# Kernel optimization log

Hardware: AMD Instinct MI355X
Metric: run time of the kernel (lower is better)

The kernel has to match this reference:

```python
import jax, jax.numpy as jnp
import numpy as np

B, T, S, H, NH, F = 16, 512, 512, 1024, 16, 4096
HD = H // NH


def _mha(x, bias, mem, wq, bq, wk, bk, wv, bv, wo, bo):
    # THUMT MultiHeadAttention: q scaled by head_dim**-0.5, additive bias on logits
    b, t, h = x.shape
    q = (x @ wq + bq) * (HD ** -0.5)
    k = mem @ wk + bk
    v = mem @ wv + bv
    split = lambda z: z.reshape(z.shape[0], z.shape[1], NH, HD).transpose(0, 2, 1, 3)
    logits = jnp.einsum('bhqd,bhkd->bhqk', split(q), split(k)) + bias
    w = jax.nn.softmax(logits, axis=-1)
    o = jnp.einsum('bhqk,bhkd->bhqd', w, split(v))
    o = o.transpose(0, 2, 1, 3).reshape(b, t, h)
    return o @ wo + bo


def _lstm(inp, w, b):
    # inp: [B, T, 2H]; gates affine over concat([x_t, h], -1): [3H] -> [4H]
    bsz = inp.shape[0]
    def step(carry, xt):
        c, hdd = carry
        g = jnp.concatenate([xt, hdd], axis=-1) @ w + b
        i, j, f, o = jnp.split(g, 4, axis=-1)
        new_c = jax.nn.sigmoid(f) * c + jax.nn.sigmoid(i) * jnp.tanh(j)
        new_h = jax.nn.sigmoid(o) * jnp.tanh(new_c)
        return (new_c, new_h), new_h
    init = (jnp.zeros((bsz, H), inp.dtype), jnp.zeros((bsz, H), inp.dtype))
    _, hs = jax.lax.scan(step, init, inp.transpose(1, 0, 2))  # [T,B,H]
    return hs.transpose(1, 0, 2)


def setup_inputs() -> dict:
    key = jax.random.key(0)
    ks = jax.random.split(key, 16)
    d = {}
    d['x'] = jax.random.normal(ks[0], (B, T, H), jnp.float32)
    d['memory'] = jax.random.normal(ks[1], (B, S, H), jnp.float32)
    d['src_bias'] = jnp.zeros((B, 1, 1, S), jnp.float32)
    causal = jnp.triu(jnp.full((T, T), -1e9, jnp.float32), k=1)
    d['tgt_bias'] = causal[None, None]
    sc = 0.02
    names = ['src_wq', 'src_wk', 'src_wv', 'src_wo', 'tgt_wq', 'tgt_wk', 'tgt_wv', 'tgt_wo']
    for i, n in enumerate(names):
        d[n] = jax.random.normal(ks[2 + i], (H, H), jnp.float32) * sc
        d[n.replace('w', 'b')] = jnp.zeros((H,), jnp.float32)
    d['lstm_w'] = jax.random.normal(ks[10], (3 * H, 4 * H), jnp.float32) * sc
    d['lstm_b'] = jnp.zeros((4 * H,), jnp.float32)
    d['ffn_w1'] = jax.random.normal(ks[11], (H, F), jnp.float32) * sc
    d['ffn_b1'] = jnp.zeros((F,), jnp.float32)
    d['ffn_w2'] = jax.random.normal(ks[12], (F, H), jnp.float32) * sc
    d['ffn_b2'] = jnp.zeros((H,), jnp.float32)
    return d


def reference(x, memory, src_bias, tgt_bias,
              src_wq, src_bq, src_wk, src_bk, src_wv, src_bv, src_wo, src_bo,
              tgt_wq, tgt_bq, tgt_wk, tgt_bk, tgt_wv, tgt_bv, tgt_wo, tgt_bo,
              lstm_w, lstm_b, ffn_w1, ffn_b1, ffn_w2, ffn_b2):
    c_src = _mha(x, src_bias, memory, src_wq, src_bq, src_wk, src_bk, src_wv, src_bv, src_wo, src_bo)
    c_tgt = _mha(x, tgt_bias, x, tgt_wq, tgt_bq, tgt_wk, tgt_bk, tgt_wv, tgt_bv, tgt_wo, tgt_bo)
    c = c_src + c_tgt  # comb_mode='sum'
    hiddens = _lstm(jnp.concatenate([x, c], axis=-1), lstm_w, lstm_b)
    hiddens = jax.nn.relu(hiddens @ ffn_w1 + ffn_b1) @ ffn_w2 + ffn_b2  # FeedForward
    return hiddens  # dropout is identity in eval
```

## Files before the change

### kernel.cpp

```cpp
#include <hip/hip_runtime.h>
#include <hip/hip_bf16.h>
#include <stdint.h>


typedef unsigned short u16;
typedef unsigned int u32;
typedef unsigned long long u64;
typedef __bf16 bf16x8 __attribute__((ext_vector_type(8)));
typedef float f32x4 __attribute__((ext_vector_type(4)));
typedef int int32x4 __attribute__((ext_vector_type(4)));
typedef unsigned long long u64x2 __attribute__((ext_vector_type(2)));

#define DEV static __device__ __forceinline__

DEV u16 f2bf(float x) {
  u32 u = __builtin_bit_cast(u32, x);
  u += 0x7FFF + ((u >> 16) & 1);
  return (u16)(u >> 16);
}

DEV bf16x8 ldfrag(const void* p) {
  int32x4 v = *(const int32x4*)p;
  return __builtin_bit_cast(bf16x8, v);
}

DEV bf16x8 mkfrag(u64 lo, u64 hi) {
  u64x2 v;
  v.x = lo;
  v.y = hi;
  return __builtin_bit_cast(bf16x8, v);
}

DEV f32x4 mfma_bf16(bf16x8 a, bf16x8 b, f32x4 c) {
  return __builtin_amdgcn_mfma_f32_16x16x32_bf16(a, b, c, 0, 0, 0);
}

DEV void load_lds16(const u16* g, u16* l) {
  __builtin_amdgcn_global_load_lds(
      (__attribute__((address_space(1))) void*)(uintptr_t)g,
      (__attribute__((address_space(3))) void*)(uintptr_t)l, 16, 0, 0);
}


__global__ __launch_bounds__(256) void cvt_bf16_kernel(u16* __restrict__ out,
                                                       const float* __restrict__ in,
                                                       int n4) {
  int i = blockIdx.x * 256 + threadIdx.x;
  if (i >= n4) return;
  float4 v = ((const float4*)in)[i];
  ushort4 s;
  s.x = f2bf(v.x); s.y = f2bf(v.y); s.z = f2bf(v.z); s.w = f2bf(v.w);
  ((ushort4*)out)[i] = s;
}

__global__ __launch_bounds__(256) void cvt_x_kernel(u16* __restrict__ out,
                                                    const float* __restrict__ in) {
  int i = blockIdx.x * 256 + threadIdx.x;
  int r = i >> 8, cg4 = i & 255;
  float4 v = ((const float4*)in)[i];
  ushort4 s;
  s.x = f2bf(v.x); s.y = f2bf(v.y); s.z = f2bf(v.z); s.w = f2bf(v.w);
  *(ushort4*)(out + (size_t)r * 2048 + cg4 * 4) = s;
}

__global__ __launch_bounds__(256) void convt_kernel(u16* __restrict__ out,
                                                    const float* __restrict__ in,
                                                    int K, int N, int koff, float scale) {
  __shared__ float tile[32][33];
  const int tid = threadIdx.x;
  const int n0 = blockIdx.x * 32, k0 = blockIdx.y * 32;
  const int c = tid & 31, r = tid >> 5;
#pragma unroll
  for (int i = 0; i < 4; ++i)
    tile[r + i * 8][c] = in[(size_t)(k0 + r + i * 8 + koff) * N + n0 + c];
  __syncthreads();
#pragma unroll
  for (int i = 0; i < 4; ++i)
    out[(size_t)(n0 + r + i * 8) * K + k0 + c] = f2bf(tile[c][r + i * 8] * scale);
}

__global__ __launch_bounds__(256) void convt_perm_kernel(u16* __restrict__ out,
                                                         const float* __restrict__ in,
                                                         int K, int koff) {
  __shared__ float tile[32][33];
  const int tid = threadIdx.x;
  const int u0 = blockIdx.x * 32, k0 = blockIdx.y * 32, g = blockIdx.z;
  const int c = tid & 31, r = tid >> 5;
#pragma unroll
  for (int i = 0; i < 4; ++i)
    tile[r + i * 8][c] = in[(size_t)(k0 + r + i * 8 + koff) * 4096 + g * 1024 + u0 + c];
  __syncthreads();
#pragma unroll
  for (int i = 0; i < 4; ++i)
    out[(size_t)((u0 + r + i * 8) * 4 + g) * K + k0 + c] = f2bf(tile[c][r + i * 8]);
}

__global__ __launch_bounds__(256) void pack_bias_kernel(float* __restrict__ out,
                                                        const float* __restrict__ in) {
  int p = blockIdx.x * 256 + threadIdx.x;
  out[p] = in[(p & 3) * 1024 + (p >> 2)];
}

template <int OUTBF, int ACCUM, int RELU, int PERM>
__global__ __launch_bounds__(256) void gemm_bt_kernel(
    const u16* __restrict__ A, int lda, const u16* __restrict__ Bt,
    const float* __restrict__ bias, float bscale,
    void* __restrict__ outp, int ostride,
    const float* __restrict__ cacc, int cstride, int K) {
  __shared__ u16 As[128 * 32];
  __shared__ u16 Bs[128 * 32];
  const int tid = threadIdx.x;
  const int wave = tid >> 6, lane = tid & 63;
  const int lr = lane & 15, lg = lane >> 4;
  const int m0 = blockIdx.y * 128, n0 = blockIdx.x * 128;
  const int wr = (wave >> 1) * 64, wc = (wave & 1) * 64;

  f32x4 acc[4][4] = {};

  const int sr = lane >> 2, sce = (lane & 3) * 8;
  const u16* gA = A + (size_t)(m0 + wave * 16 + sr) * lda + sce;
  const u16* gB = Bt + (size_t)(n0 + wave * 16 + sr) * K + sce;
  u16* lA = As + wave * 16 * 32;
  u16* lB = Bs + wave * 16 * 32;

  for (int k0 = 0; k0 < K; k0 += 32) {
    __syncthreads();
    load_lds16(gA + k0, lA);
    load_lds16(gA + k0 + (size_t)64 * lda, lA + 64 * 32);
    load_lds16(gB + k0, lB);
    load_lds16(gB + k0 + (size_t)64 * K, lB + 64 * 32);
    __syncthreads();
    bf16x8 af[4], bfr[4];
    const u16* pa = As + (wr + lr) * 32 + lg * 8;
    const u16* pb = Bs + (wc + lr) * 32 + lg * 8;
#pragma unroll
    for (int i = 0; i < 4; ++i) af[i] = ldfrag(pa + i * 16 * 32);
#pragma unroll
    for (int j = 0; j < 4; ++j) bfr[j] = ldfrag(pb + j * 16 * 32);
#pragma unroll
    for (int i = 0; i < 4; ++i)
#pragma unroll
      for (int j = 0; j < 4; ++j)
        acc[i][j] = mfma_bf16(af[i], bfr[j], acc[i][j]);
  }

  const int col0 = n0 + wc + lr;
  const int row0 = m0 + wr + lg * 4;
#pragma unroll
  for (int i = 0; i < 4; ++i) {
#pragma unroll
    for (int j = 0; j < 4; ++j) {
      const int c = col0 + j * 16;
      const float bv = bias ? bias[c] * bscale : 0.f;
#pragma unroll
      for (int ii = 0; ii < 4; ++ii) {
        const int r = row0 + i * 16 + ii;
        float v = acc[i][j][ii] + bv;
        if (ACCUM) v += cacc[(size_t)r * cstride + c];
        if (RELU) v = fmaxf(v, 0.f);
        const int rp = (PERM == 2) ? ((r & 15) * 512 + (r >> 4)) : r;
        if (OUTBF) ((u16*)outp)[(size_t)rp * ostride + c] = f2bf(v);
        else       ((float*)outp)[(size_t)rp * ostride + c] = v;
      }
    }
  }
}

template <int CAUSAL>
__global__ __launch_bounds__(256) void flash_kernel(
    const u16* __restrict__ Q, const u16* __restrict__ Kb, const u16* __restrict__ Vb,
    const float* __restrict__ sbias, u16* __restrict__ O) {
  __shared__ u16 Kl[64 * 72];
  __shared__ u16 Vt[64 * 72];
  __shared__ u16 Pl[64 * 72];
  const int tid = threadIdx.x, wave = tid >> 6, lane = tid & 63;
  const int lr = lane & 15, lg = lane >> 4;
  const int q0 = blockIdx.x * 64, hh = blockIdx.y, b = blockIdx.z;

  bf16x8 qf[2];
  {
    const u16* qp = Q + (size_t)(b * 512 + q0 + wave * 16 + lr) * 1024 + hh * 64 + lg * 8;
    qf[0] = ldfrag(qp);
    qf[1] = ldfrag(qp + 32);
  }
  f32x4 oacc[4] = {};
  float mrun[4], lsum[4];
#pragma unroll
  for (int ii = 0; ii < 4; ++ii) { mrun[ii] = -3e38f; lsum[ii] = 0.f; }

  const int ntiles = CAUSAL ? (q0 / 64 + 1) : 8;
  for (int ti = 0; ti < ntiles; ++ti) {
    const int s0 = ti * 64;
    {
      const int r = tid >> 2, ch = (tid & 3) * 16;
      const u16* kp = Kb + (size_t)(b * 512 + s0 + r) * 1024 + hh * 64 + ch;
      const u16* vp = Vb + (size_t)(b * 512 + s0 + r) * 1024 + hh * 64 + ch;
      int32x4 k0v = *(const int32x4*)kp;
      int32x4 k1v = *(const int32x4*)(kp + 8);
      int32x4 v0v = *(const int32x4*)vp;
      int32x4 v1v = *(const int32x4*)(vp + 8);
      *(int32x4*)&Kl[r * 72 + ch] = k0v;
      *(int32x4*)&Kl[r * 72 + ch + 8] = k1v;
      const u16* v0p = (const u16*)&v0v;
      const u16* v1p = (const u16*)&v1v;
#pragma unroll
      for (int j = 0; j < 8; ++j) {
        Vt[(ch + j) * 72 + r] = v0p[j];
        Vt[(ch + 8 + j) * 72 + r] = v1p[j];
      }
    }
    __syncthreads();
    f32x4 sf[4] = {};
#pragma unroll
    for (int j = 0; j < 4; ++j)
#pragma unroll
      for (int ks = 0; ks < 2; ++ks) {
        bf16x8 kf = ldfrag(&Kl[(j * 16 + lr) * 72 + ks * 32 + lg * 8]);
        sf[j] = mfma_bf16(qf[ks], kf, sf[j]);
      }
    if (!CAUSAL) {
#pragma unroll
      for (int j = 0; j < 4; ++j) {
        const float bv = sbias[b * 512 + s0 + j * 16 + lr];
#pragma unroll
        for (int ii = 0; ii < 4; ++ii) sf[j][ii] += bv;
      }
    } else {
#pragma unroll
      for (int j = 0; j < 4; ++j) {
        const int s = s0 + j * 16 + lr;
#pragma unroll
        for (int ii = 0; ii < 4; ++ii) {
          const int q = q0 + wave * 16 + lg * 4 + ii;
          if (s > q) sf[j][ii] -= 1e9f;
        }
      }
    }
    float sc[4], rs[4];
#pragma unroll
    for (int ii = 0; ii < 4; ++ii) {
      float m = fmaxf(fmaxf(sf[0][ii], sf[1][ii]), fmaxf(sf[2][ii], sf[3][ii]));
#pragma unroll
      for (int off = 1; off < 16; off <<= 1) m = fmaxf(m, __shfl_xor(m, off));
      const float mn = fmaxf(mrun[ii], m);
      sc[ii] = __expf(mrun[ii] - mn);
      mrun[ii] = mn;
      rs[ii] = 0.f;
    }
#pragma unroll
    for (int j = 0; j < 4; ++j)
#pragma unroll
      for (int ii = 0; ii < 4; ++ii) {
        const float p = __expf(sf[j][ii] - mrun[ii]);
        rs[ii] += p;
        Pl[(wave * 16 + lg * 4 + ii) * 72 + j * 16 + lr] = f2bf(p);
      }
#pragma unroll
    for (int ii = 0; ii < 4; ++ii) {
      float r = rs[ii];
#pragma unroll
      for (int off = 1; off < 16; off <<= 1) r += __shfl_xor(r, off);
      lsum[ii] = lsum[ii] * sc[ii] + r;
    }
#pragma unroll
    for (int df = 0; df < 4; ++df)
#pragma unroll
      for (int ii = 0; ii < 4; ++ii) oacc[df][ii] *= sc[ii];
    __syncthreads();
    bf16x8 pf[2];
    pf[0] = ldfrag(&Pl[(wave * 16 + lr) * 72 + lg * 8]);
    pf[1] = ldfrag(&Pl[(wave * 16 + lr) * 72 + 32 + lg * 8]);
#pragma unroll
    for (int df = 0; df < 4; ++df)
#pragma unroll
      for (int ks = 0; ks < 2; ++ks) {
        bf16x8 vf = ldfrag(&Vt[(df * 16 + lr) * 72 + ks * 32 + lg * 8]);
        oacc[df] = mfma_bf16(pf[ks], vf, oacc[df]);
      }
    __syncthreads();
  }
#pragma unroll
  for (int df = 0; df < 4; ++df)
#pragma unroll
    for (int ii = 0; ii < 4; ++ii) {
      const float v = oacc[df][ii] / lsum[ii];
      O[(size_t)(b * 512 + q0 + wave * 16 + lg * 4 + ii) * 1024 + hh * 64 + df * 16 + lr] =
          f2bf(v);
    }
}

#define SCAN_NW 32
__global__ __launch_bounds__(256, 1) void lstm_scan_kernel(
    const u16* __restrict__ Whp, const float* __restrict__ gx,
    u16* __restrict__ hbuf) {
  const int tid = threadIdx.x, wave = tid >> 6, lane = tid & 63;
  const int lr = lane & 15, lg = lane >> 4;
  const int g = blockIdx.x;
  __shared__ float part[2][4][16][128];
  const int gb = tid >> 4;
  const int up = tid & 15;
  float cs0 = 0.f, cs1 = 0.f;
  const u64 SENT = 0xFFFFFFFFFFFFFFFFull;

  const u16* wbase = Whp + (size_t)(g * 128 + lr) * 1024 + wave * 256 + lg * 8;
  const float* gxp = gx + (size_t)gb * 512 * 4096 + g * 128 + up * 8;

  for (int t = 0; t < 512; ++t) {
    const float4 gxv0 = *(const float4*)(gxp + (size_t)t * 4096);
    const float4 gxv1 = *(const float4*)(gxp + (size_t)t * 4096 + 4);
    const u16* hp = hbuf + (size_t)t * 16384 + lr * 1024 + wave * 256 + lg * 8;
    u64 hw[16];
#pragma unroll
    for (int kc = 0; kc < 8; ++kc) {
      hw[kc * 2] = __hip_atomic_load((const u64*)(hp + kc * 32),
                                     __ATOMIC_RELAXED, __HIP_MEMORY_SCOPE_AGENT);
      hw[kc * 2 + 1] = __hip_atomic_load((const u64*)(hp + kc * 32 + 4),
                                         __ATOMIC_RELAXED, __HIP_MEMORY_SCOPE_AGENT);
    }
    {
      int guard = 0;
      for (;;) {
        bool ok = true;
#pragma unroll
        for (int i = 0; i < 16; ++i) ok &= (hw[i] != SENT);
        if (__all((int)ok)) break;
        __builtin_amdgcn_s_sleep(4);
        if (++guard > (1 << 20)) break;
#pragma unroll
        for (int kc = 0; kc < 8; ++kc) {
          if (hw[kc * 2] == SENT)
            hw[kc * 2] = __hip_atomic_load((const u64*)(hp + kc * 32),
                                           __ATOMIC_RELAXED, __HIP_MEMORY_SCOPE_AGENT);
          if (hw[kc * 2 + 1] == SENT)
            hw[kc * 2 + 1] = __hip_atomic_load((const u64*)(hp + kc * 32 + 4),
                                               __ATOMIC_RELAXED, __HIP_MEMORY_SCOPE_AGENT);
        }
      }
    }
    f32x4 acc[8] = {};
#pragma unroll
    for (int kc = 0; kc < 8; ++kc) {
      const bf16x8 hf = mkfrag(hw[kc * 2], hw[kc * 2 + 1]);
#pragma unroll
      for (int j = 0; j < 8; ++j)
        acc[j] = mfma_bf16(hf, ldfrag(wbase + j * 16 * 1024 + kc * 32), acc[j]);
    }
    const int p = t & 1;
#pragma unroll
    for (int j = 0; j < 8; ++j)
#pragma unroll
      for (int ii = 0; ii < 4; ++ii)
        part[p][wave][lg * 4 + ii][j * 16 + lr] = acc[j][ii];
    __syncthreads();
    float s[8];
#pragma unroll
    for (int k = 0; k < 8; ++k)
      s[k] = part[p][0][gb][up * 8 + k] + part[p][1][gb][up * 8 + k] +
             part[p][2][gb][up * 8 + k] + part[p][3][gb][up * 8 + k];
    float hA, hB;
    {
      const float si = s[0] + gxv0.x, sj = s[1] + gxv0.y;
      const float sf_ = s[2] + gxv0.z, so = s[3] + gxv0.w;
      const float ig = 1.f / (1.f + __expf(-si));
      const float jg = 1.f - 2.f / (__expf(2.f * sj) + 1.f);
      const float fg = 1.f / (1.f + __expf(-sf_));
      const float og = 1.f / (1.f + __expf(-so));
      cs0 = fg * cs0 + ig * jg;
      hA = og * (1.f - 2.f / (__expf(2.f * cs0) + 1.f));
    }
    {
      const float si = s[4] + gxv1.x, sj = s[5] + gxv1.y;
      const float sf_ = s[6] + gxv1.z, so = s[7] + gxv1.w;
      const float ig = 1.f / (1.f + __expf(-si));
      const float jg = 1.f - 2.f / (__expf(2.f * sj) + 1.f);
      const float fg = 1.f / (1.f + __expf(-sf_));
      const float og = 1.f / (1.f + __expf(-so));
      cs1 = fg * cs1 + ig * jg;
      hB = og * (1.f - 2.f / (__expf(2.f * cs1) + 1.f));
    }
    const u32 myw = (u32)f2bf(hA) | ((u32)f2bf(hB) << 16);
    const u32 otherw = (u32)__shfl_down((int)myw, 1);
    if (!(up & 1)) {
      u64 w64 = (u64)myw | ((u64)otherw << 32);
      u64* dst = (u64*)(hbuf + (size_t)(t + 1) * 16384 + gb * 1024 + g * 32 + up * 2);
      __hip_atomic_store(dst, w64, __ATOMIC_RELAXED, __HIP_MEMORY_SCOPE_AGENT);
    }
  }
}


extern "C" void kernel_launch(void* const* d_in, const int* in_sizes, int n_in,
                              void* d_out, int out_size, void* d_ws, size_t ws_size,
                              hipStream_t stream) {
  const float* x        = (const float*)d_in[0];
  const float* mem      = (const float*)d_in[1];
  const float* src_bias = (const float*)d_in[2];
  const float* w_src_q = (const float*)d_in[4];  const float* b_src_q = (const float*)d_in[5];
  const float* w_src_k = (const float*)d_in[6];  const float* b_src_k = (const float*)d_in[7];
  const float* w_src_v = (const float*)d_in[8];  const float* b_src_v = (const float*)d_in[9];
  const float* w_src_o = (const float*)d_in[10]; const float* b_src_o = (const float*)d_in[11];
  const float* w_tgt_q = (const float*)d_in[12]; const float* b_tgt_q = (const float*)d_in[13];
  const float* w_tgt_k = (const float*)d_in[14]; const float* b_tgt_k = (const float*)d_in[15];
  const float* w_tgt_v = (const float*)d_in[16]; const float* b_tgt_v = (const float*)d_in[17];
  const float* w_tgt_o = (const float*)d_in[18]; const float* b_tgt_o = (const float*)d_in[19];
  const float* lstm_w  = (const float*)d_in[20]; const float* lstm_b  = (const float*)d_in[21];
  const float* w1 = (const float*)d_in[22]; const float* b1f = (const float*)d_in[23];
  const float* w2 = (const float*)d_in[24]; const float* b2f = (const float*)d_in[25];

  char* ws = (char*)d_ws;
  const size_t MiB = 1024ull * 1024ull;
  u16*   xcb  = (u16*)(ws + 0);
  u16*   wlp  = (u16*)(ws + 32 * MiB);
  u16*   whp  = (u16*)(ws + 48 * MiB);
  u16*   w1t  = (u16*)(ws + 56 * MiB);
  u16*   w2t  = (u16*)(ws + 64 * MiB);
  float* pb   = (float*)(ws + 72 * MiB);
  u16*   hbuf = (u16*)(ws + 73 * MiB);
  u16*   memb = (u16*)(ws + 90 * MiB);
  u16*   wt[8];
  for (int i = 0; i < 8; ++i) wt[i] = (u16*)(ws + 106 * MiB + (size_t)i * 2 * MiB);
  u16*   bq   = (u16*)(ws + 122 * MiB);
  u16*   bk   = (u16*)(ws + 138 * MiB);
  u16*   bv   = (u16*)(ws + 154 * MiB);
  u16*   ao_s = (u16*)(ws + 170 * MiB);
  u16*   ao_t = (u16*)(ws + 186 * MiB);
  float* c32  = (float*)(ws + 202 * MiB);
  float* gx   = (float*)(ws + 90 * MiB);
  u16*   ffn1 = (u16*)(ws + 90 * MiB);

  hipMemsetAsync(hbuf + 16384, 0xFF, (size_t)512 * 16384 * 2, stream);
  hipMemsetAsync(hbuf, 0, 32768, stream);

  cvt_x_kernel<<<8192, 256, 0, stream>>>(xcb, x);
  cvt_bf16_kernel<<<8192, 256, 0, stream>>>(memb, mem, 2097152);
  const dim3 g1k(32, 32);
  convt_kernel<<<g1k, 256, 0, stream>>>(wt[0], w_src_q, 1024, 1024, 0, 0.125f);
  convt_kernel<<<g1k, 256, 0, stream>>>(wt[1], w_src_k, 1024, 1024, 0, 1.f);
  convt_kernel<<<g1k, 256, 0, stream>>>(wt[2], w_src_v, 1024, 1024, 0, 1.f);
  convt_kernel<<<g1k, 256, 0, stream>>>(wt[3], w_src_o, 1024, 1024, 0, 1.f);
  convt_kernel<<<g1k, 256, 0, stream>>>(wt[4], w_tgt_q, 1024, 1024, 0, 0.125f);
  convt_kernel<<<g1k, 256, 0, stream>>>(wt[5], w_tgt_k, 1024, 1024, 0, 1.f);
  convt_kernel<<<g1k, 256, 0, stream>>>(wt[6], w_tgt_v, 1024, 1024, 0, 1.f);
  convt_kernel<<<g1k, 256, 0, stream>>>(wt[7], w_tgt_o, 1024, 1024, 0, 1.f);
  convt_perm_kernel<<<dim3(32, 64, 4), 256, 0, stream>>>(wlp, lstm_w, 2048, 0);
  convt_perm_kernel<<<dim3(32, 32, 4), 256, 0, stream>>>(whp, lstm_w, 1024, 2048);
  convt_kernel<<<dim3(128, 32), 256, 0, stream>>>(w1t, w1, 1024, 4096, 0, 1.f);
  convt_kernel<<<dim3(32, 128), 256, 0, stream>>>(w2t, w2, 4096, 1024, 0, 1.f);
  pack_bias_kernel<<<16, 256, 0, stream>>>(pb, lstm_b);

  const dim3 gN1(8, 64);
  const dim3 gN4(32, 64);

  gemm_bt_kernel<1, 0, 0, 0><<<gN1, 256, 0, stream>>>(xcb, 2048, wt[0], b_src_q, 0.125f, bq, 1024, nullptr, 0, 1024);
  gemm_bt_kernel<1, 0, 0, 0><<<gN1, 256, 0, stream>>>(memb, 1024, wt[1], b_src_k, 1.f, bk, 1024, nullptr, 0, 1024);
  gemm_bt_kernel<1, 0, 0, 0><<<gN1, 256, 0, stream>>>(memb, 1024, wt[2], b_src_v, 1.f, bv, 1024, nullptr, 0, 1024);
  flash_kernel<0><<<dim3(8, 16, 16), 256, 0, stream>>>(bq, bk, bv, src_bias, ao_s);
  gemm_bt_kernel<1, 0, 0, 0><<<gN1, 256, 0, stream>>>(xcb, 2048, wt[4], b_tgt_q, 0.125f, bq, 1024, nullptr, 0, 1024);
  gemm_bt_kernel<1, 0, 0, 0><<<gN1, 256, 0, stream>>>(xcb, 2048, wt[5], b_tgt_k, 1.f, bk, 1024, nullptr, 0, 1024);
  gemm_bt_kernel<1, 0, 0, 0><<<gN1, 256, 0, stream>>>(xcb, 2048, wt[6], b_tgt_v, 1.f, bv, 1024, nullptr, 0, 1024);
  flash_kernel<1><<<dim3(8, 16, 16), 256, 0, stream>>>(bq, bk, bv, nullptr, ao_t);
  gemm_bt_kernel<0, 0, 0, 0><<<gN1, 256, 0, stream>>>(ao_s, 1024, wt[3], b_src_o, 1.f, c32, 1024, nullptr, 0, 1024);
  gemm_bt_kernel<1, 1, 0, 0><<<gN1, 256, 0, stream>>>(ao_t, 1024, wt[7], b_tgt_o, 1.f, xcb + 1024, 2048, c32, 1024, 1024);
  gemm_bt_kernel<0, 0, 0, 0><<<gN4, 256, 0, stream>>>(xcb, 2048, wlp, pb, 1.f, gx, 4096, nullptr, 0, 2048);
  lstm_scan_kernel<<<dim3(SCAN_NW), 256, 0, stream>>>(whp, gx, hbuf);
  gemm_bt_kernel<1, 0, 1, 0><<<gN4, 256, 0, stream>>>(hbuf + 16384, 1024, w1t, b1f, 1.f, ffn1, 4096, nullptr, 0, 1024);
  gemm_bt_kernel<0, 0, 0, 2><<<gN1, 256, 0, stream>>>(ffn1, 4096, w2t, b2f, 1.f, (float*)d_out, 1024, nullptr, 0, 4096);
}
```

Before: 3.002 ms.

## Split LSTM scan batch into two halves and pipeline h loads with MFMA

```diff
diff --git a/kernel.cpp b/kernel.cpp
--- a/kernel.cpp
+++ b/kernel.cpp
@@ -296,96 +296,113 @@
   const int tid = threadIdx.x, wave = tid >> 6, lane = tid & 63;
   const int lr = lane & 15, lg = lane >> 4;
   const int g = blockIdx.x;
-  __shared__ float part[2][4][16][128];
-  const int gb = tid >> 4;
-  const int up = tid & 15;
-  float cs0 = 0.f, cs1 = 0.f;
+  __shared__ float part[2][4][8][132];
+  const int gb = tid >> 5;
+  const int uu = tid & 31;
+  float csA = 0.f, csB = 0.f;
   const u64 SENT = 0xFFFFFFFFFFFFFFFFull;
 
   const u16* wbase = Whp + (size_t)(g * 128 + lr) * 1024 + wave * 256 + lg * 8;
-  const float* gxp = gx + (size_t)gb * 512 * 4096 + g * 128 + up * 8;
-
+  const float* gxpA = gx + (size_t)gb * 512 * 4096 + g * 128 + uu * 4;
+  const float* gxpB = gxpA + (size_t)8 * 512 * 4096;
+  const size_t goffA = (size_t)(lr & 7) * 1024 + wave * 256 + lg * 8;
+  const size_t goffB = goffA + 8 * 1024;
+
+  u64 hwA[16], hwB[16];
+#define ISSUE(hw, base, t)                                                        \
+  {                                                                               \
+    const u16* hp_ = hbuf + (size_t)(t) * 16384 + (base);                         \
+    _Pragma("unroll") for (int kc = 0; kc < 8; ++kc) {                            \
+      hw[kc * 2] = __hip_atomic_load((const u64*)(hp_ + kc * 32),                 \
+                                     __ATOMIC_RELAXED, __HIP_MEMORY_SCOPE_AGENT); \
+      hw[kc * 2 + 1] = __hip_atomic_load((const u64*)(hp_ + kc * 32 + 4),         \
+                                         __ATOMIC_RELAXED,                       \
+                                         __HIP_MEMORY_SCOPE_AGENT);              \
+    }                                                                             \
+  }
+#define SPINFIX(hw, base, t)                                                      \
+  {                                                                               \
+    const u16* hp_ = hbuf + (size_t)(t) * 16384 + (base);                         \
+    int guard_ = 0;                                                               \
+    for (;;) {                                                                    \
+      bool ok_ = true;                                                            \
+      _Pragma("unroll") for (int i = 0; i < 16; ++i) ok_ &= (hw[i] != SENT);      \
+      if (__all((int)ok_)) break;                                                 \
+      __builtin_amdgcn_s_sleep(2);                                                \
+      if (++guard_ > (1 << 20)) break;                                            \
+      _Pragma("unroll") for (int kc = 0; kc < 8; ++kc) {                          \
+        if (hw[kc * 2] == SENT)                                                   \
+          hw[kc * 2] = __hip_atomic_load((const u64*)(hp_ + kc * 32),             \
+                                         __ATOMIC_RELAXED,                       \
+                                         __HIP_MEMORY_SCOPE_AGENT);              \
+        if (hw[kc * 2 + 1] == SENT)                                               \
+          hw[kc * 2 + 1] = __hip_atomic_load((const u64*)(hp_ + kc * 32 + 4),     \
+                                             __ATOMIC_RELAXED,                   \
+                                             __HIP_MEMORY_SCOPE_AGENT);          \
+      }                                                                           \
+    }                                                                             \
+  }
+#define MFMA_PART(grp, hw)                                                        \
+  {                                                                               \
+    f32x4 acc_[8] = {};                                                           \
+    _Pragma("unroll") for (int kc = 0; kc < 8; ++kc) {                            \
+      const bf16x8 hf_ = mkfrag(hw[kc * 2], hw[kc * 2 + 1]);                      \
+      _Pragma("unroll") for (int j = 0; j < 8; ++j)                               \
+          acc_[j] = mfma_bf16(hf_, ldfrag(wbase + j * 16 * 1024 + kc * 32),       \
+                              acc_[j]);                                           \
+    }                                                                             \
+    if (lg < 2) {                                                                 \
+      _Pragma("unroll") for (int j = 0; j < 8; ++j)                               \
+          _Pragma("unroll") for (int ii = 0; ii < 4; ++ii)                        \
+          part[grp][wave][lg * 4 + ii][j * 16 + lr] = acc_[j][ii];                \
+    }                                                                             \
+  }
+#define GATES_PUB(grp, cs, gxv, bglob, t)                                         \
+  {                                                                               \
+    float4 s_ = *(const float4*)&part[grp][0][gb][uu * 4];                        \
+    _Pragma("unroll") for (int w_ = 1; w_ < 4; ++w_) {                            \
+      const float4 v_ = *(const float4*)&part[grp][w_][gb][uu * 4];               \
+      s_.x += v_.x; s_.y += v_.y; s_.z += v_.z; s_.w += v_.w;                     \
+    }                                                                             \
+    const float si_ = s_.x + gxv.x, sj_ = s_.y + gxv.y;                           \
+    const float sf_ = s_.z + gxv.z, so_ = s_.w + gxv.w;                           \
+    const float ig_ = 1.f / (1.f + __expf(-si_));                                 \
+    const float jg_ = 1.f - 2.f / (__expf(2.f * sj_) + 1.f);                      \
+    const float fg_ = 1.f / (1.f + __expf(-sf_));                                 \
+    const float og_ = 1.f / (1.f + __expf(-so_));                                 \
+    cs = fg_ * cs + ig_ * jg_;                                                    \
+    const float hn_ = og_ * (1.f - 2.f / (__expf(2.f * cs) + 1.f));               \
+    const u32 w16_ = (u32)f2bf(hn_);                                              \
+    const u32 p2_ = w16_ | ((u32)__shfl_down((int)w16_, 1) << 16);                \
+    const u64 p4_ = (u64)p2_ | ((u64)(u32)__shfl_down((int)p2_, 2) << 32);        \
+    if ((uu & 3) == 0) {                                                          \
+      u64* dst_ = (u64*)(hbuf + (size_t)((t) + 1) * 16384 + (size_t)(bglob) * 1024 \
+                         + g * 32 + uu);                                          \
+      __hip_atomic_store(dst_, p4_, __ATOMIC_RELAXED, __HIP_MEMORY_SCOPE_AGENT);  \
+    }                                                                             \
+  }
+
+  ISSUE(hwA, goffA, 0);
   for (int t = 0; t < 512; ++t) {
-    const float4 gxv0 = *(const float4*)(gxp + (size_t)t * 4096);
-    const float4 gxv1 = *(const float4*)(gxp + (size_t)t * 4096 + 4);
-    const u16* hp = hbuf + (size_t)t * 16384 + lr * 1024 + wave * 256 + lg * 8;
-    u64 hw[16];
-#pragma unroll
-    for (int kc = 0; kc < 8; ++kc) {
-      hw[kc * 2] = __hip_atomic_load((const u64*)(hp + kc * 32),
-                                     __ATOMIC_RELAXED, __HIP_MEMORY_SCOPE_AGENT);
-      hw[kc * 2 + 1] = __hip_atomic_load((const u64*)(hp + kc * 32 + 4),
-                                         __ATOMIC_RELAXED, __HIP_MEMORY_SCOPE_AGENT);
-    }
-    {
-      int guard = 0;
-      for (;;) {
-        bool ok = true;
-#pragma unroll
-        for (int i = 0; i < 16; ++i) ok &= (hw[i] != SENT);
-        if (__all((int)ok)) break;
-        __builtin_amdgcn_s_sleep(4);
-        if (++guard > (1 << 20)) break;
-#pragma unroll
-        for (int kc = 0; kc < 8; ++kc) {
-          if (hw[kc * 2] == SENT)
-            hw[kc * 2] = __hip_atomic_load((const u64*)(hp + kc * 32),
-                                           __ATOMIC_RELAXED, __HIP_MEMORY_SCOPE_AGENT);
-          if (hw[kc * 2 + 1] == SENT)
-            hw[kc * 2 + 1] = __hip_atomic_load((const u64*)(hp + kc * 32 + 4),
-                                               __ATOMIC_RELAXED, __HIP_MEMORY_SCOPE_AGENT);
-        }
-      }
-    }
-    f32x4 acc[8] = {};
-#pragma unroll
-    for (int kc = 0; kc < 8; ++kc) {
-      const bf16x8 hf = mkfrag(hw[kc * 2], hw[kc * 2 + 1]);
-#pragma unroll
-      for (int j = 0; j < 8; ++j)
-        acc[j] = mfma_bf16(hf, ldfrag(wbase + j * 16 * 1024 + kc * 32), acc[j]);
-    }
-    const int p = t & 1;
-#pragma unroll
-    for (int j = 0; j < 8; ++j)
-#pragma unroll
-      for (int ii = 0; ii < 4; ++ii)
-        part[p][wave][lg * 4 + ii][j * 16 + lr] = acc[j][ii];
-    __syncthreads();
-    float s[8];
-#pragma unroll
-    for (int k = 0; k < 8; ++k)
-      s[k] = part[p][0][gb][up * 8 + k] + part[p][1][gb][up * 8 + k] +
-             part[p][2][gb][up * 8 + k] + part[p][3][gb][up * 8 + k];
-    float hA, hB;
-    {
-      const float si = s[0] + gxv0.x, sj = s[1] + gxv0.y;
-      const float sf_ = s[2] + gxv0.z, so = s[3] + gxv0.w;
-      const float ig = 1.f / (1.f + __expf(-si));
-      const float jg = 1.f - 2.f / (__expf(2.f * sj) + 1.f);
-      const float fg = 1.f / (1.f + __expf(-sf_));
-      const float og = 1.f / (1.f + __expf(-so));
-      cs0 = fg * cs0 + ig * jg;
-      hA = og * (1.f - 2.f / (__expf(2.f * cs0) + 1.f));
-    }
-    {
-      const float si = s[4] + gxv1.x, sj = s[5] + gxv1.y;
-      const float sf_ = s[6] + gxv1.z, so = s[7] + gxv1.w;
-      const float ig = 1.f / (1.f + __expf(-si));
-      const float jg = 1.f - 2.f / (__expf(2.f * sj) + 1.f);
-      const float fg = 1.f / (1.f + __expf(-sf_));
-      const float og = 1.f / (1.f + __expf(-so));
-      cs1 = fg * cs1 + ig * jg;
-      hB = og * (1.f - 2.f / (__expf(2.f * cs1) + 1.f));
-    }
-    const u32 myw = (u32)f2bf(hA) | ((u32)f2bf(hB) << 16);
-    const u32 otherw = (u32)__shfl_down((int)myw, 1);
-    if (!(up & 1)) {
-      u64 w64 = (u64)myw | ((u64)otherw << 32);
-      u64* dst = (u64*)(hbuf + (size_t)(t + 1) * 16384 + gb * 1024 + g * 32 + up * 2);
-      __hip_atomic_store(dst, w64, __ATOMIC_RELAXED, __HIP_MEMORY_SCOPE_AGENT);
-    }
-  }
+    const float4 gxvA = *(const float4*)(gxpA + (size_t)t * 4096);
+    const float4 gxvB = *(const float4*)(gxpB + (size_t)t * 4096);
+    SPINFIX(hwA, goffA, t);
+    ISSUE(hwB, goffB, t);
+    __builtin_amdgcn_sched_barrier(0);
+    MFMA_PART(0, hwA);
+    __syncthreads();
+    GATES_PUB(0, csA, gxvA, gb, t);
+    SPINFIX(hwB, goffB, t);
+    if (t + 1 < 512) ISSUE(hwA, goffA, t + 1);
+    __builtin_amdgcn_sched_barrier(0);
+    MFMA_PART(1, hwB);
+    __syncthreads();
+    GATES_PUB(1, csB, gxvB, gb + 8, t);
+  }
+#undef ISSUE
+#undef SPINFIX
+#undef MFMA_PART
+#undef GATES_PUB
 }
 
 
```

Result: slower. 4.538 ms (+51.2%).

## Overlap FFN first GEMM with LSTM scan via worker blocks polling hidden states

Applied to the files above, without the earlier changes.

```diff
diff --git a/kernel.cpp b/kernel.cpp
--- a/kernel.cpp
+++ b/kernel.cpp
@@ -33,6 +33,10 @@
 
 DEV f32x4 mfma_bf16(bf16x8 a, bf16x8 b, f32x4 c) {
   return __builtin_amdgcn_mfma_f32_16x16x32_bf16(a, b, c, 0, 0, 0);
+}
+
+DEV u64 aload(const u64* p) {
+  return __hip_atomic_load(p, __ATOMIC_RELAXED, __HIP_MEMORY_SCOPE_AGENT);
 }
 
 DEV void load_lds16(const u16* g, u16* l) {
@@ -106,7 +110,7 @@
     const u16* __restrict__ A, int lda, const u16* __restrict__ Bt,
     const float* __restrict__ bias, float bscale,
     void* __restrict__ outp, int ostride,
-    const float* __restrict__ cacc, int cstride, int K) {
+    const float* __restrict__ cacc, int cstride, int K, int moff) {
   __shared__ u16 As[128 * 32];
   __shared__ u16 Bs[128 * 32];
   const int tid = threadIdx.x;
@@ -158,7 +162,8 @@
         float v = acc[i][j][ii] + bv;
         if (ACCUM) v += cacc[(size_t)r * cstride + c];
         if (RELU) v = fmaxf(v, 0.f);
-        const int rp = (PERM == 2) ? ((r & 15) * 512 + (r >> 4)) : r;
+        const int gr = moff + r;
+        const int rp = (PERM == 2) ? ((gr & 15) * 512 + (gr >> 4)) : r;
         if (OUTBF) ((u16*)outp)[(size_t)rp * ostride + c] = f2bf(v);
         else       ((float*)outp)[(size_t)rp * ostride + c] = v;
       }
@@ -290,100 +295,194 @@
 }
 
 #define SCAN_NW 32
+#define NWORK 192
 __global__ __launch_bounds__(256, 1) void lstm_scan_kernel(
     const u16* __restrict__ Whp, const float* __restrict__ gx,
-    u16* __restrict__ hbuf) {
+    u16* __restrict__ hbuf, const u16* __restrict__ w1t,
+    const float* __restrict__ b1f, u16* __restrict__ f0, u16* __restrict__ f1) {
   const int tid = threadIdx.x, wave = tid >> 6, lane = tid & 63;
   const int lr = lane & 15, lg = lane >> 4;
   const int g = blockIdx.x;
-  __shared__ float part[2][4][16][128];
-  const int gb = tid >> 4;
-  const int up = tid & 15;
-  float cs0 = 0.f, cs1 = 0.f;
+  __shared__ float part[2][4][16][132];
   const u64 SENT = 0xFFFFFFFFFFFFFFFFull;
 
-  const u16* wbase = Whp + (size_t)(g * 128 + lr) * 1024 + wave * 256 + lg * 8;
-  const float* gxp = gx + (size_t)gb * 512 * 4096 + g * 128 + up * 8;
-
-  for (int t = 0; t < 512; ++t) {
-    const float4 gxv0 = *(const float4*)(gxp + (size_t)t * 4096);
-    const float4 gxv1 = *(const float4*)(gxp + (size_t)t * 4096 + 4);
-    const u16* hp = hbuf + (size_t)t * 16384 + lr * 1024 + wave * 256 + lg * 8;
+  if (g < SCAN_NW) {
+    const int gb = tid >> 4;
+    const int up = tid & 15;
+    float cs0 = 0.f, cs1 = 0.f;
+    const u16* wbase = Whp + (size_t)(g * 128 + lr) * 1024 + wave * 256 + lg * 8;
+    const float* gxp = gx + (size_t)gb * 512 * 4096 + g * 128 + up * 8;
+    const size_t goff = (size_t)lr * 1024 + wave * 256 + lg * 8;
+
     u64 hw[16];
-#pragma unroll
-    for (int kc = 0; kc < 8; ++kc) {
-      hw[kc * 2] = __hip_atomic_load((const u64*)(hp + kc * 32),
-                                     __ATOMIC_RELAXED, __HIP_MEMORY_SCOPE_AGENT);
-      hw[kc * 2 + 1] = __hip_atomic_load((const u64*)(hp + kc * 32 + 4),
-                                         __ATOMIC_RELAXED, __HIP_MEMORY_SCOPE_AGENT);
-    }
-    {
-      int guard = 0;
-      for (;;) {
-        bool ok = true;
-#pragma unroll
-        for (int i = 0; i < 16; ++i) ok &= (hw[i] != SENT);
-        if (__all((int)ok)) break;
-        __builtin_amdgcn_s_sleep(4);
-        if (++guard > (1 << 20)) break;
-#pragma unroll
-        for (int kc = 0; kc < 8; ++kc) {
-          if (hw[kc * 2] == SENT)
-            hw[kc * 2] = __hip_atomic_load((const u64*)(hp + kc * 32),
-                                           __ATOMIC_RELAXED, __HIP_MEMORY_SCOPE_AGENT);
-          if (hw[kc * 2 + 1] == SENT)
-            hw[kc * 2 + 1] = __hip_atomic_load((const u64*)(hp + kc * 32 + 4),
-                                               __ATOMIC_RELAXED, __HIP_MEMORY_SCOPE_AGENT);
+#define ISSUE(t)                                                               \
+  {                                                                            \
+    const u16* hp_ = hbuf + (size_t)(t) * 16384 + goff;                        \
+    _Pragma("unroll") for (int kc = 0; kc < 8; ++kc) {                         \
+      hw[kc * 2] = aload((const u64*)(hp_ + kc * 32));                         \
+      hw[kc * 2 + 1] = aload((const u64*)(hp_ + kc * 32 + 4));                 \
+    }                                                                          \
+  }
+#define SPINFIX(t)                                                             \
+  {                                                                            \
+    const u16* hp_ = hbuf + (size_t)(t) * 16384 + goff;                        \
+    int guard_ = 0;                                                            \
+    for (;;) {                                                                 \
+      bool ok_ = true;                                                         \
+      _Pragma("unroll") for (int i = 0; i < 16; ++i) ok_ &= (hw[i] != SENT);   \
+      if (__all((int)ok_)) break;                                              \
+      __builtin_amdgcn_s_sleep(2);                                             \
+      if (++guard_ > (1 << 20)) break;                                         \
+      _Pragma("unroll") for (int kc = 0; kc < 8; ++kc) {                       \
+        if (hw[kc * 2] == SENT)                                                \
+          hw[kc * 2] = aload((const u64*)(hp_ + kc * 32));                     \
+        if (hw[kc * 2 + 1] == SENT)                                            \
+          hw[kc * 2 + 1] = aload((const u64*)(hp_ + kc * 32 + 4));             \
+      }                                                                        \
+    }                                                                          \
+  }
+
+    ISSUE(0);
+    float4 gxv0 = *(const float4*)gxp;
+    float4 gxv1 = *(const float4*)(gxp + 4);
+    for (int t = 0; t < 512; ++t) {
+      float4 gxn0, gxn1;
+      if (t + 1 < 512) {
+        gxn0 = *(const float4*)(gxp + (size_t)(t + 1) * 4096);
+        gxn1 = *(const float4*)(gxp + (size_t)(t + 1) * 4096 + 4);
+      }
+      SPINFIX(t);
+      f32x4 acc[8] = {};
+#pragma unroll
+      for (int kc = 0; kc < 8; ++kc) {
+        const bf16x8 hf = mkfrag(hw[kc * 2], hw[kc * 2 + 1]);
+#pragma unroll
+        for (int j = 0; j < 8; ++j)
+          acc[j] = mfma_bf16(hf, ldfrag(wbase + j * 16 * 1024 + kc * 32), acc[j]);
+      }
+      const int p = t & 1;
+#pragma unroll
+      for (int j = 0; j < 8; ++j)
+#pragma unroll
+        for (int ii = 0; ii < 4; ++ii)
+          part[p][wave][lg * 4 + ii][j * 16 + lr] = acc[j][ii];
+      __syncthreads();
+      float4 sA = *(const float4*)&part[p][0][gb][up * 8];
+      float4 sB = *(const float4*)&part[p][0][gb][up * 8 + 4];
+#pragma unroll
+      for (int w = 1; w < 4; ++w) {
+        const float4 a = *(const float4*)&part[p][w][gb][up * 8];
+        const float4 b = *(const float4*)&part[p][w][gb][up * 8 + 4];
+        sA.x += a.x; sA.y += a.y; sA.z += a.z; sA.w += a.w;
+        sB.x += b.x; sB.y += b.y; sB.z += b.z; sB.w += b.w;
+      }
+      float hA, hB;
+      {
+        const float si = sA.x + gxv0.x, sj = sA.y + gxv0.y;
+        const float sf_ = sA.z + gxv0.z, so = sA.w + gxv0.w;
+        const float ig = 1.f / (1.f + __expf(-si));
+        const float jg = 1.f - 2.f / (__expf(2.f * sj) + 1.f);
+        const float fg = 1.f / (1.f + __expf(-sf_));
+        const float og = 1.f / (1.f + __expf(-so));
+        cs0 = fg * cs0 + ig * jg;
+        hA = og * (1.f - 2.f / (__expf(2.f * cs0) + 1.f));
+      }
+      {
+        const float si = sB.x + gxv1.x, sj = sB.y + gxv1.y;
+        const float sf_ = sB.z + gxv1.z, so = sB.w + gxv1.w;
+        const float ig = 1.f / (1.f + __expf(-si));
+        const float jg = 1.f - 2.f / (__expf(2.f * sj) + 1.f);
+        const float fg = 1.f / (1.f + __expf(-sf_));
+        const float og = 1.f / (1.f + __expf(-so));
+        cs1 = fg * cs1 + ig * jg;
+        hB = og * (1.f - 2.f / (__expf(2.f * cs1) + 1.f));
+      }
+      const u32 myw = (u32)f2bf(hA) | ((u32)f2bf(hB) << 16);
+      const u32 otherw = (u32)__shfl_down((int)myw, 1);
+      if (!(up & 1)) {
+        u64 w64 = (u64)myw | ((u64)otherw << 32);
+        u64* dst = (u64*)(hbuf + (size_t)(t + 1) * 16384 + (size_t)gb * 1024 +
+                          g * 32 + up * 2);
+        __hip_atomic_store(dst, w64, __ATOMIC_RELAXED, __HIP_MEMORY_SCOPE_AGENT);
+      }
+      ISSUE(t + 1);
+      gxv0 = gxn0;
+      gxv1 = gxn1;
+    }
+#undef ISSUE
+#undef SPINFIX
+  } else {
+    const int wk = g - SCAN_NW;
+    u16* As = (u16*)&part[0][0][0][0];
+    u16* Bs = As + 128 * 32;
+    const int wr = (wave >> 1) * 64, wc = (wave & 1) * 64;
+    for (int idx = wk; idx < 2048; idx += NWORK) {
+      const int mi = idx >> 5, ni = idx & 31;
+      const u16* Arows = hbuf + 16384 + (size_t)mi * 131072;
+      if (wave == 0) {
+        const u64* pr = (const u64*)(Arows + 112 * 1024) + (size_t)lane * 32;
+        u64 v[32];
+#pragma unroll
+        for (int i = 0; i < 32; ++i) v[i] = aload(pr + i);
+        int guard = 0;
+        for (;;) {
+          bool ok = true;
+#pragma unroll
+          for (int i = 0; i < 32; ++i) ok &= (v[i] != SENT);
+          if (__all((int)ok)) break;
+          __builtin_amdgcn_s_sleep(64);
+          if (++guard > (1 << 22)) break;
+#pragma unroll
+          for (int i = 0; i < 32; ++i)
+            if (v[i] == SENT) v[i] = aload(pr + i);
         }
       }
-    }
-    f32x4 acc[8] = {};
-#pragma unroll
-    for (int kc = 0; kc < 8; ++kc) {
-      const bf16x8 hf = mkfrag(hw[kc * 2], hw[kc * 2 + 1]);
-#pragma unroll
-      for (int j = 0; j < 8; ++j)
-        acc[j] = mfma_bf16(hf, ldfrag(wbase + j * 16 * 1024 + kc * 32), acc[j]);
-    }
-    const int p = t & 1;
-#pragma unroll
-    for (int j = 0; j < 8; ++j)
-#pragma unroll
-      for (int ii = 0; ii < 4; ++ii)
-        part[p][wave][lg * 4 + ii][j * 16 + lr] = acc[j][ii];
-    __syncthreads();
-    float s[8];
-#pragma unroll
-    for (int k = 0; k < 8; ++k)
-      s[k] = part[p][0][gb][up * 8 + k] + part[p][1][gb][up * 8 + k] +
-             part[p][2][gb][up * 8 + k] + part[p][3][gb][up * 8 + k];
-    float hA, hB;
-    {
-      const float si = s[0] + gxv0.x, sj = s[1] + gxv0.y;
-      const float sf_ = s[2] + gxv0.z, so = s[3] + gxv0.w;
-      const float ig = 1.f / (1.f + __expf(-si));
-      const float jg = 1.f - 2.f / (__expf(2.f * sj) + 1.f);
-      const float fg = 1.f / (1.f + __expf(-sf_));
-      const float og = 1.f / (1.f + __expf(-so));
-      cs0 = fg * cs0 + ig * jg;
-      hA = og * (1.f - 2.f / (__expf(2.f * cs0) + 1.f));
-    }
-    {
-      const float si = s[4] + gxv1.x, sj = s[5] + gxv1.y;
-      const float sf_ = s[6] + gxv1.z, so = s[7] + gxv1.w;
-      const float ig = 1.f / (1.f + __expf(-si));
-      const float jg = 1.f - 2.f / (__expf(2.f * sj) + 1.f);
-      const float fg = 1.f / (1.f + __expf(-sf_));
-      const float og = 1.f / (1.f + __expf(-so));
-      cs1 = fg * cs1 + ig * jg;
-      hB = og * (1.f - 2.f / (__expf(2.f * cs1) + 1.f));
-    }
-    const u32 myw = (u32)f2bf(hA) | ((u32)f2bf(hB) << 16);
-    const u32 otherw = (u32)__shfl_down((int)myw, 1);
-    if (!(up & 1)) {
-      u64 w64 = (u64)myw | ((u64)otherw << 32);
-      u64* dst = (u64*)(hbuf + (size_t)(t + 1) * 16384 + gb * 1024 + g * 32 + up * 2);
-      __hip_atomic_store(dst, w64, __ATOMIC_RELAXED, __HIP_MEMORY_SCOPE_AGENT);
+      __syncthreads();
+      f32x4 acc[4][4] = {};
+      const int sr = lane >> 2, sce = (lane & 3) * 8;
+      const u16* gA = Arows + (size_t)(wave * 16 + sr) * 1024 + sce;
+      const u16* gB = w1t + (size_t)(ni * 128 + wave * 16 + sr) * 1024 + sce;
+      u16* lA = As + wave * 16 * 32;
+      u16* lB = Bs + wave * 16 * 32;
+      for (int k0 = 0; k0 < 1024; k0 += 32) {
+        __syncthreads();
+        load_lds16(gA + k0, lA);
+        load_lds16(gA + k0 + 64 * 1024, lA + 64 * 32);
+        load_lds16(gB + k0, lB);
+        load_lds16(gB + k0 + 64 * 1024, lB + 64 * 32);
+        __syncthreads();
+        bf16x8 af[4], bfr[4];
+        const u16* pa = As + (wr + lr) * 32 + lg * 8;
+        const u16* pb = Bs + (wc + lr) * 32 + lg * 8;
+#pragma unroll
+        for (int i = 0; i < 4; ++i) af[i] = ldfrag(pa + i * 16 * 32);
+#pragma unroll
+        for (int j = 0; j < 4; ++j) bfr[j] = ldfrag(pb + j * 16 * 32);
+#pragma unroll
+        for (int i = 0; i < 4; ++i)
+#pragma unroll
+          for (int j = 0; j < 4; ++j)
+            acc[i][j] = mfma_bf16(af[i], bfr[j], acc[i][j]);
+      }
+      const int col0 = ni * 128 + wc + lr;
+      const int row0 = mi * 128 + wr + lg * 4;
+#pragma unroll
+      for (int i = 0; i < 4; ++i) {
+#pragma unroll
+        for (int j = 0; j < 4; ++j) {
+          const int c = col0 + j * 16;
+          const float bv = b1f[c];
+#pragma unroll
+          for (int ii = 0; ii < 4; ++ii) {
+            const int R = row0 + i * 16 + ii;
+            const float v = fmaxf(acc[i][j][ii] + bv, 0.f);
+            u16* ob = (R < 6144) ? (f0 + (size_t)R * 4096)
+                                 : (f1 + (size_t)(R - 6144) * 4096);
+            ob[c] = f2bf(v);
+          }
+        }
+      }
+      __syncthreads();
     }
   }
 }
@@ -426,7 +525,8 @@
   u16*   ao_t = (u16*)(ws + 186 * MiB);
   float* c32  = (float*)(ws + 202 * MiB);
   float* gx   = (float*)(ws + 90 * MiB);
-  u16*   ffn1 = (u16*)(ws + 90 * MiB);
+  u16*   f0   = (u16*)(ws + 0);
+  u16*   f1   = (u16*)(ws + 218 * MiB);
 
   hipMemsetAsync(hbuf + 16384, 0xFF, (size_t)512 * 16384 * 2, stream);
   hipMemsetAsync(hbuf, 0, 32768, stream);
@@ -451,18 +551,19 @@
   const dim3 gN1(8, 64);
   const dim3 gN4(32, 64);
 
-  gemm_bt_kernel<1, 0, 0, 0><<<gN1, 256, 0, stream>>>(xcb, 2048, wt[0], b_src_q, 0.125f, bq, 1024, nullptr, 0, 1024);
-  gemm_bt_kernel<1, 0, 0, 0><<<gN1, 256, 0, stream>>>(memb, 1024, wt[1], b_src_k, 1.f, bk, 1024, nullptr, 0, 1024);
-  gemm_bt_kernel<1, 0, 0, 0><<<gN1, 256, 0, stream>>>(memb, 1024, wt[2], b_src_v, 1.f, bv, 1024, nullptr, 0, 1024);
+  gemm_bt_kernel<1, 0, 0, 0><<<gN1, 256, 0, stream>>>(xcb, 2048, wt[0], b_src_q, 0.125f, bq, 1024, nullptr, 0, 1024, 0);
+  gemm_bt_kernel<1, 0, 0, 0><<<gN1, 256, 0, stream>>>(memb, 1024, wt[1], b_src_k, 1.f, bk, 1024, nullptr, 0, 1024, 0);
+  gemm_bt_kernel<1, 0, 0, 0><<<gN1, 256, 0, stream>>>(memb, 1024, wt[2], b_src_v, 1.f, bv, 1024, nullptr, 0, 1024, 0);
   flash_kernel<0><<<dim3(8, 16, 16), 256, 0, stream>>>(bq, bk, bv, src_bias, ao_s);
-  gemm_bt_kernel<1, 0, 0, 0><<<gN1, 256, 0, stream>>>(xcb, 2048, wt[4], b_tgt_q, 0.125f, bq, 1024, nullptr, 0, 1024);
-  gemm_bt_kernel<1, 0, 0, 0><<<gN1, 256, 0, stream>>>(xcb, 2048, wt[5], b_tgt_k, 1.f, bk, 1024, nullptr, 0, 1024);
-  gemm_bt_kernel<1, 0, 0, 0><<<gN1, 256, 0, stream>>>(xcb, 2048, wt[6], b_tgt_v, 1.f, bv, 1024, nullptr, 0, 1024);
+  gemm_bt_kernel<1, 0, 0, 0><<<gN1, 256, 0, stream>>>(xcb, 2048, wt[4], b_tgt_q, 0.125f, bq, 1024, nullptr, 0, 1024, 0);
+  gemm_bt_kernel<1, 0, 0, 0><<<gN1, 256, 0, stream>>>(xcb, 2048, wt[5], b_tgt_k, 1.f, bk, 1024, nullptr, 0, 1024, 0);
+  gemm_bt_kernel<1, 0, 0, 0><<<gN1, 256, 0, stream>>>(xcb, 2048, wt[6], b_tgt_v, 1.f, bv, 1024, nullptr, 0, 1024, 0);
   flash_kernel<1><<<dim3(8, 16, 16), 256, 0, stream>>>(bq, bk, bv, nullptr, ao_t);
-  gemm_bt_kernel<0, 0, 0, 0><<<gN1, 256, 0, stream>>>(ao_s, 1024, wt[3], b_src_o, 1.f, c32, 1024, nullptr, 0, 1024);
-  gemm_bt_kernel<1, 1, 0, 0><<<gN1, 256, 0, stream>>>(ao_t, 1024, wt[7], b_tgt_o, 1.f, xcb + 1024, 2048, c32, 1024, 1024);
-  gemm_bt_kernel<0, 0, 0, 0><<<gN4, 256, 0, stream>>>(xcb, 2048, wlp, pb, 1.f, gx, 4096, nullptr, 0, 2048);
-  lstm_scan_kernel<<<dim3(SCAN_NW), 256, 0, stream>>>(whp, gx, hbuf);
-  gemm_bt_kernel<1, 0, 1, 0><<<gN4, 256, 0, stream>>>(hbuf + 16384, 1024, w1t, b1f, 1.f, ffn1, 4096, nullptr, 0, 1024);
-  gemm_bt_kernel<0, 0, 0, 2><<<gN1, 256, 0, stream>>>(ffn1, 4096, w2t, b2f, 1.f, (float*)d_out, 1024, nullptr, 0, 4096);
-}
+  gemm_bt_kernel<0, 0, 0, 0><<<gN1, 256, 0, stream>>>(ao_s, 1024, wt[3], b_src_o, 1.f, c32, 1024, nullptr, 0, 1024, 0);
+  gemm_bt_kernel<1, 1, 0, 0><<<gN1, 256, 0, stream>>>(ao_t, 1024, wt[7], b_tgt_o, 1.f, xcb + 1024, 2048, c32, 1024, 1024, 0);
+  gemm_bt_kernel<0, 0, 0, 0><<<gN4, 256, 0, stream>>>(xcb, 2048, wlp, pb, 1.f, gx, 4096, nullptr, 0, 2048, 0);
+  lstm_scan_kernel<<<dim3(SCAN_NW + NWORK), 256, 14336, stream>>>(
+      whp, gx, hbuf, w1t, b1f, f0, f1);
+  gemm_bt_kernel<0, 0, 0, 2><<<dim3(8, 48), 256, 0, stream>>>(f0, 4096, w2t, b2f, 1.f, (float*)d_out, 1024, nullptr, 0, 4096, 0);
+  gemm_bt_kernel<0, 0, 0, 2><<<dim3(8, 16), 256, 0, stream>>>(f1, 4096, w2t, b2f, 1.f, (float*)d_out, 1024, nullptr, 0, 4096, 6144);
+}
```

After: 3.251 ms. 8.3% more time.
